# Kernel optimization log

Measured on AMD Instinct MI355X. Metric: run time of the kernel, lower is better.

Reference implementation:

```python
import jax, jax.numpy as jnp
import numpy as np

B, H, W = 64, 512, 512          # batch, image height/width
BH, BW = 8, 8                   # block_size
K = 256                         # n_blocks (codebook size)
L = BH * BW                     # block_len = 64
HT, WT = H // BH, W // BW       # tiles per axis
T = HT * WT                     # tiles_per_img = 4096
BETA = 35.0


def _unfold(img):
    # img: (B, 1, H, W) -> patches (B, T, L), matching torch.nn.Unfold
    # with kernel=stride=(BH,BW): tiles row-major, patch flattened (kh, kw).
    x = img.reshape(B, 1, HT, BH, WT, BW)
    x = x.transpose(0, 2, 4, 1, 3, 5)          # (B, HT, WT, 1, BH, BW)
    return x.reshape(B, T, L)


def _fold(patches):
    # patches: (B, T, L) -> img (B, 1, H, W); exact inverse of _unfold
    # (non-overlapping, so Fold is pure reassembly, no accumulation).
    x = patches.reshape(B, HT, WT, 1, BH, BW)
    x = x.transpose(0, 3, 1, 4, 2, 5)          # (B, 1, HT, BH, WT, BW)
    return x.reshape(B, 1, H, W)


def setup_inputs() -> dict:
    key = jax.random.key(0)
    k1, k2 = jax.random.split(key)
    target_img = jax.random.uniform(k1, (B, 1, H, W), dtype=jnp.float32)
    # Learned codebook parameter (Haar-ish init in the original; values
    # don't change the math being tested).
    blocks = jax.random.uniform(k2, (K, BH, BW), dtype=jnp.float32)
    return {"target_img": target_img, "blocks": blocks}


def reference(target_img, blocks):
    patches = _unfold(target_img).reshape(B * T, L)   # (N, L), N = B*T
    codes = blocks.reshape(K, L)                      # (K, L)

    # Squared distances ||a - b||^2 via the expanded form to avoid
    # materializing the (N, K, L) difference tensor.
    a2 = jnp.sum(patches * patches, axis=-1, keepdims=True)   # (N, 1)
    b2 = jnp.sum(codes * codes, axis=-1)                      # (K,)
    ab = patches @ codes.T                                    # (N, K)
    sqerr = a2 - 2.0 * ab + b2                                # (N, K)

    block_weights = jax.nn.softmax(-BETA * sqerr, axis=-1)    # (N, K)
    uf_reconstructed = block_weights @ codes                  # (N, L)

    reconstructed = _fold(uf_reconstructed.reshape(B, T, L))  # (B,1,H,W)
    choice_penalty = jnp.mean(
        jnp.minimum(block_weights, 1.0 - block_weights)) * K
    return reconstructed, choice_penalty
```

## Files before the change

kernel.cpp:

```cpp
#include <hip/hip_runtime.h>


typedef short short8 __attribute__((ext_vector_type(8)));
typedef float floatx4 __attribute__((ext_vector_type(4)));

namespace {
constexpr float BETA_C = 35.0f;
constexpr float TAU    = 1e-6f;
constexpr float INV_N  = 1.0f / 262144.0f;
constexpr size_t IMG_ELEMS = (size_t)64 * 512 * 512;
constexpr int WR = 0;
constexpr int WS = 4352;
constexpr int NWORDS = 4416;
}

__device__ __forceinline__ unsigned short f2bf(float x) {
  unsigned u = __float_as_uint(x);
  return (unsigned short)((u + 0x7FFFu + ((u >> 16) & 1u)) >> 16);
}
__device__ __forceinline__ float bf2f(unsigned short h) {
  return __uint_as_float((unsigned)h << 16);
}
__device__ __forceinline__ unsigned pack2(unsigned short lo, unsigned short hi) {
  return (unsigned)lo | ((unsigned)hi << 16);
}
__device__ __forceinline__ void cvt8t(float4 a, float4 b, short8& h, short8& l) {
  float f[8] = {a.x, a.y, a.z, a.w, b.x, b.y, b.z, b.w};
#pragma unroll
  for (int i = 0; i < 8; ++i) {
    unsigned short hh = f2bf(f[i]);
    h[i] = (short)hh;
    float lf = f[i] - bf2f(hh);
    l[i] = (short)(__float_as_uint(lf) >> 16);
  }
}
__device__ __forceinline__ int swz(int j) {
  return (j & ~7) | ((j ^ (j >> 3)) & 7);
}

__global__ void pack_codes(const float* __restrict__ blk,
                           unsigned* __restrict__ wsBh,
                           unsigned* __restrict__ wsBl,
                           float* __restrict__ wsB2) {
  const int c = threadIdx.x;
  const float* src = blk + c * 64;
  float b2 = 0.f;
#pragma unroll
  for (int g = 0; g < 8; ++g) {
#pragma unroll
    for (int t = 0; t < 4; ++t) {
      float v0 = src[g * 8 + 2 * t], v1 = src[g * 8 + 2 * t + 1];
      b2 += v0 * v0 + v1 * v1;
      unsigned short h0 = f2bf(v0), h1 = f2bf(v1);
      unsigned short l0 = f2bf(v0 - bf2f(h0)), l1 = f2bf(v1 - bf2f(h1));
      wsBh[(c * 8 + g) * 4 + t] = pack2(h0, h1);
      wsBl[(c * 8 + g) * 4 + t] = pack2(l0, l1);
    }
  }
  wsB2[c] = b2;
}

__global__ __launch_bounds__(256, 5) void recon_kernel(
    const float* __restrict__ img, const float* __restrict__ blk,
    const unsigned* __restrict__ wsBh, const unsigned* __restrict__ wsBl,
    const float* __restrict__ wsB2, float* __restrict__ out,
    float* __restrict__ penAcc) {
  __shared__ unsigned sMem[NWORDS];
  float* sMemF = reinterpret_cast<float*>(sMem);
  uint4* sMem4 = reinterpret_cast<uint4*>(sMem);

  const int tid = threadIdx.x;
  const int lane = tid & 63;
  const int wave = tid >> 6;
  const int b = blockIdx.x >> 6;
  const int ht = blockIdx.x & 63;
  const int c15 = lane & 15;
  const int q = lane >> 4;

  const float* imgBase = img + (size_t)b * (512 * 512) + (size_t)(ht * 8) * 512;
  const float* aptr = imgBase + q * 512 + (wave * 16 + c15) * 8;
  float4 v00 = *reinterpret_cast<const float4*>(aptr);
  float4 v01 = *reinterpret_cast<const float4*>(aptr + 4);
  float4 v10 = *reinterpret_cast<const float4*>(aptr + 2048);
  float4 v11 = *reinterpret_cast<const float4*>(aptr + 2048 + 4);

  uint4 tH[4], tL[4];
  {
    const uint4* src = reinterpret_cast<const uint4*>(wsBh);
#pragma unroll
    for (int i = 0; i < 4; ++i) tH[i] = src[swz(i * 256 + tid)];
  }

  short8 ah[2], al[2];
  cvt8t(v00, v01, ah[0], al[0]);
  cvt8t(v10, v11, ah[1], al[1]);

  const int kx = c15 & 7;
  const unsigned* pb0 = &sMem[(8 * c15 + (q ^ kx)) * 4];
  const unsigned* pb1 = &sMem[(8 * c15 + ((q ^ 4) ^ kx)) * 4];

  float m[4], sm[4];
  float rr[16] = {0.f, 0.f, 0.f, 0.f, 0.f, 0.f, 0.f, 0.f,
                  0.f, 0.f, 0.f, 0.f, 0.f, 0.f, 0.f, 0.f};

#pragma unroll
  for (int h = 0; h < 2; ++h) {
    if (h == 1) __syncthreads();
#pragma unroll
    for (int i = 0; i < 4; ++i) sMem4[i * 256 + tid] = tH[i];
    __syncthreads();
    {
      const uint4* src = reinterpret_cast<const uint4*>(wsBl) + h * 1024;
#pragma unroll
      for (int i = 0; i < 4; ++i) tL[i] = src[swz(i * 256 + tid)];
    }
    floatx4 acc[8];
#pragma unroll
    for (int n = 0; n < 8; ++n) acc[n] = (floatx4){0.f, 0.f, 0.f, 0.f};
#pragma unroll
    for (int n = 0; n < 8; ++n) {
      short8 b0 = *reinterpret_cast<const short8*>(pb0 + 512 * n);
      short8 b1 = *reinterpret_cast<const short8*>(pb1 + 512 * n);
      acc[n] = __builtin_amdgcn_mfma_f32_16x16x32_bf16(ah[0], b0, acc[n], 0, 0, 0);
      acc[n] = __builtin_amdgcn_mfma_f32_16x16x32_bf16(al[0], b0, acc[n], 0, 0, 0);
      acc[n] = __builtin_amdgcn_mfma_f32_16x16x32_bf16(ah[1], b1, acc[n], 0, 0, 0);
      acc[n] = __builtin_amdgcn_mfma_f32_16x16x32_bf16(al[1], b1, acc[n], 0, 0, 0);
    }
    __syncthreads();
#pragma unroll
    for (int i = 0; i < 4; ++i) sMem4[i * 256 + tid] = tL[i];
    __syncthreads();
    if (h == 0) {
      const uint4* src = reinterpret_cast<const uint4*>(wsBh) + 1024;
#pragma unroll
      for (int i = 0; i < 4; ++i) tH[i] = src[swz(i * 256 + tid)];
    }
#pragma unroll
    for (int n = 0; n < 8; ++n) {
      short8 b0 = *reinterpret_cast<const short8*>(pb0 + 512 * n);
      short8 b1 = *reinterpret_cast<const short8*>(pb1 + 512 * n);
      acc[n] = __builtin_amdgcn_mfma_f32_16x16x32_bf16(ah[0], b0, acc[n], 0, 0, 0);
      acc[n] = __builtin_amdgcn_mfma_f32_16x16x32_bf16(ah[1], b1, acc[n], 0, 0, 0);
    }

#pragma unroll
    for (int n = 0; n < 8; ++n) {
      float b2v = wsB2[128 * h + 16 * n + c15];
#pragma unroll
      for (int r = 0; r < 4; ++r)
        acc[n][r] = fmaf(2.0f * BETA_C, acc[n][r], -BETA_C * b2v);
    }
    float M[4];
#pragma unroll
    for (int r = 0; r < 4; ++r) {
      float mm = acc[0][r];
#pragma unroll
      for (int n = 1; n < 8; ++n) mm = fmaxf(mm, acc[n][r]);
#pragma unroll
      for (int off = 1; off <= 8; off <<= 1) mm = fmaxf(mm, __shfl_xor(mm, off, 64));
      M[r] = mm;
    }
    if (h == 0) {
#pragma unroll
      for (int r = 0; r < 4; ++r) { m[r] = M[r]; sm[r] = 0.f; }
    } else {
      float scl[4];
#pragma unroll
      for (int r = 0; r < 4; ++r) {
        float mn = fmaxf(m[r], M[r]);
        scl[r] = __expf(m[r] - mn);
        m[r] = mn;
        sm[r] *= scl[r];
      }
#pragma unroll
      for (int qq = 0; qq < 4; ++qq)
#pragma unroll
        for (int r = 0; r < 4; ++r) {
          float sq = __shfl(scl[r], qq * 16 + c15, 64);
          rr[4 * qq + r] *= sq;
        }
    }
#pragma unroll
    for (int n = 0; n < 8; ++n)
#pragma unroll
      for (int r = 0; r < 4; ++r) {
        float e = __expf(acc[n][r] - m[r]);
        acc[n][r] = e;
        sm[r] += e;
      }
#pragma unroll
    for (int n = 0; n < 8; ++n) {
      float em = fmaxf(fmaxf(acc[n][0], acc[n][1]), fmaxf(acc[n][2], acc[n][3]));
      unsigned long long msk = __ballot(em > TAU);
      while (msk) {
        int L = __builtin_ctzll(msk);
        msk &= msk - 1;
        float w0 = __uint_as_float(__builtin_amdgcn_readlane(__float_as_uint(acc[n][0]), L));
        float w1 = __uint_as_float(__builtin_amdgcn_readlane(__float_as_uint(acc[n][1]), L));
        float w2 = __uint_as_float(__builtin_amdgcn_readlane(__float_as_uint(acc[n][2]), L));
        float w3 = __uint_as_float(__builtin_amdgcn_readlane(__float_as_uint(acc[n][3]), L));
        float bv = blk[(size_t)(128 * h + 16 * n + (L & 15)) * 64 + lane];
        switch (L >> 4) {
          case 0: rr[0] += w0 * bv;  rr[1] += w1 * bv;  rr[2] += w2 * bv;  rr[3] += w3 * bv;  break;
          case 1: rr[4] += w0 * bv;  rr[5] += w1 * bv;  rr[6] += w2 * bv;  rr[7] += w3 * bv;  break;
          case 2: rr[8] += w0 * bv;  rr[9] += w1 * bv;  rr[10] += w2 * bv; rr[11] += w3 * bv; break;
          default: rr[12] += w0 * bv; rr[13] += w1 * bv; rr[14] += w2 * bv; rr[15] += w3 * bv; break;
        }
      }
    }
  }

  float invS[4];
#pragma unroll
  for (int r = 0; r < 4; ++r) {
#pragma unroll
    for (int off = 1; off <= 8; off <<= 1) sm[r] += __shfl_xor(sm[r], off, 64);
    invS[r] = 1.0f / sm[r];
  }
  float pen = 0.f;
  if (c15 == 0) {
#pragma unroll
    for (int r = 0; r < 4; ++r) {
      pen += (invS[r] > 0.5f) ? (2.0f - 2.0f * invS[r]) : 1.0f;
      sMemF[WS + wave * 16 + 4 * q + r] = invS[r];
    }
  }
  pen += __shfl_xor(pen, 16, 64);
  pen += __shfl_xor(pen, 32, 64);
  if (lane == 0) atomicAdd(penAcc, pen * INV_N);

  __syncthreads();

#pragma unroll
  for (int pl = 0; pl < 16; ++pl)
    sMemF[WR + (wave * 16 + pl) * 68 + lane] = rr[pl];
  float* outBase = out + (size_t)b * (512 * 512) + (size_t)(ht * 8) * 512 +
                   wave * 128;
#pragma unroll
  for (int i = 0; i < 4; ++i) {
    int f = i * 64 + lane;
    int row = f >> 5;
    int cc = f & 31;
    int wtl = cc >> 1, hw = cc & 1;
    float4 v = *reinterpret_cast<const float4*>(
        &sMemF[WR + (wave * 16 + wtl) * 68 + row * 8 + hw * 4]);
    float is = sMemF[WS + wave * 16 + wtl];
    v.x *= is; v.y *= is; v.z *= is; v.w *= is;
    *reinterpret_cast<float4*>(outBase + row * 512 + cc * 4) = v;
  }
}

extern "C" void kernel_launch(void* const* d_in, const int* in_sizes, int n_in,
                              void* d_out, int out_size, void* d_ws, size_t ws_size,
                              hipStream_t stream) {
  const float* img = (const float*)d_in[0];
  const float* blk = (const float*)d_in[1];
  float* out = (float*)d_out;
  float* penSlot = out + IMG_ELEMS;

  unsigned* wsBh = (unsigned*)d_ws;
  unsigned* wsBl = wsBh + 8192;
  float* wsB2 = (float*)(wsBl + 8192);

  pack_codes<<<dim3(1), dim3(256), 0, stream>>>(blk, wsBh, wsBl, wsB2);
  hipMemsetAsync(penSlot, 0, sizeof(float), stream);
  recon_kernel<<<dim3(4096), dim3(256), 0, stream>>>(img, blk, wsBh, wsBl,
                                                     wsB2, out, penSlot);
}
```

Before: 382.3 us.

## Stream codebook hi/lo halves directly into LDS with async global_load_lds

After: 347.2 us. 9.2% less time.

```diff
diff --git a/kernel.cpp b/kernel.cpp
--- a/kernel.cpp
+++ b/kernel.cpp
@@ -9,9 +9,11 @@
 constexpr float TAU    = 1e-6f;
 constexpr float INV_N  = 1.0f / 262144.0f;
 constexpr size_t IMG_ELEMS = (size_t)64 * 512 * 512;
-constexpr int WR = 0;
-constexpr int WS = 4352;
-constexpr int NWORDS = 4416;
+constexpr int WB0 = 0;
+constexpr int WB1 = 4096;
+constexpr int WR  = 0;
+constexpr int WS  = 4352;
+constexpr int NWORDS = 8192;
 }
 
 __device__ __forceinline__ unsigned short f2bf(float x) {
@@ -34,8 +36,10 @@
     l[i] = (short)(__float_as_uint(lf) >> 16);
   }
 }
-__device__ __forceinline__ int swz(int j) {
-  return (j & ~7) | ((j ^ (j >> 3)) & 7);
+__device__ __forceinline__ void cp16(const uint4* g, unsigned* l) {
+  __builtin_amdgcn_global_load_lds(
+      (const __attribute__((address_space(1))) void*)g,
+      (__attribute__((address_space(3))) void*)l, 16, 0, 0);
 }
 
 __global__ void pack_codes(const float* __restrict__ blk,
@@ -47,17 +51,18 @@
   float b2 = 0.f;
 #pragma unroll
   for (int g = 0; g < 8; ++g) {
+    int slot = c * 8 + (g ^ (c & 7));
 #pragma unroll
     for (int t = 0; t < 4; ++t) {
       float v0 = src[g * 8 + 2 * t], v1 = src[g * 8 + 2 * t + 1];
       b2 += v0 * v0 + v1 * v1;
       unsigned short h0 = f2bf(v0), h1 = f2bf(v1);
       unsigned short l0 = f2bf(v0 - bf2f(h0)), l1 = f2bf(v1 - bf2f(h1));
-      wsBh[(c * 8 + g) * 4 + t] = pack2(h0, h1);
-      wsBl[(c * 8 + g) * 4 + t] = pack2(l0, l1);
-    }
-  }
-  wsB2[c] = b2;
+      wsBh[slot * 4 + t] = pack2(h0, h1);
+      wsBl[slot * 4 + t] = pack2(l0, l1);
+    }
+  }
+  wsB2[c] = -BETA_C * b2;
 }
 
 __global__ __launch_bounds__(256, 5) void recon_kernel(
@@ -67,7 +72,6 @@
     float* __restrict__ penAcc) {
   __shared__ unsigned sMem[NWORDS];
   float* sMemF = reinterpret_cast<float*>(sMem);
-  uint4* sMem4 = reinterpret_cast<uint4*>(sMem);
 
   const int tid = threadIdx.x;
   const int lane = tid & 63;
@@ -84,17 +88,21 @@
   float4 v10 = *reinterpret_cast<const float4*>(aptr + 2048);
   float4 v11 = *reinterpret_cast<const float4*>(aptr + 2048 + 4);
 
-  uint4 tH[4], tL[4];
-  {
-    const uint4* src = reinterpret_cast<const uint4*>(wsBh);
-#pragma unroll
-    for (int i = 0; i < 4; ++i) tH[i] = src[swz(i * 256 + tid)];
+  const uint4* srcH = reinterpret_cast<const uint4*>(wsBh);
+  const uint4* srcL = reinterpret_cast<const uint4*>(wsBl);
+#pragma unroll
+  for (int i = 0; i < 4; ++i) {
+    cp16(srcH + i * 256 + tid, &sMem[WB0 + (i * 4 + wave) * 256]);
+    cp16(srcL + i * 256 + tid, &sMem[WB1 + (i * 4 + wave) * 256]);
   }
 
   short8 ah[2], al[2];
   cvt8t(v00, v01, ah[0], al[0]);
   cvt8t(v10, v11, ah[1], al[1]);
 
+  asm volatile("s_waitcnt vmcnt(0)" ::: "memory");
+  __syncthreads();
+
   const int kx = c15 & 7;
   const unsigned* pb0 = &sMem[(8 * c15 + (q ^ kx)) * 4];
   const unsigned* pb1 = &sMem[(8 * c15 + ((q ^ 4) ^ kx)) * 4];
@@ -105,50 +113,37 @@
 
 #pragma unroll
   for (int h = 0; h < 2; ++h) {
-    if (h == 1) __syncthreads();
-#pragma unroll
-    for (int i = 0; i < 4; ++i) sMem4[i * 256 + tid] = tH[i];
-    __syncthreads();
-    {
-      const uint4* src = reinterpret_cast<const uint4*>(wsBl) + h * 1024;
-#pragma unroll
-      for (int i = 0; i < 4; ++i) tL[i] = src[swz(i * 256 + tid)];
-    }
     floatx4 acc[8];
 #pragma unroll
     for (int n = 0; n < 8; ++n) acc[n] = (floatx4){0.f, 0.f, 0.f, 0.f};
 #pragma unroll
     for (int n = 0; n < 8; ++n) {
-      short8 b0 = *reinterpret_cast<const short8*>(pb0 + 512 * n);
-      short8 b1 = *reinterpret_cast<const short8*>(pb1 + 512 * n);
-      acc[n] = __builtin_amdgcn_mfma_f32_16x16x32_bf16(ah[0], b0, acc[n], 0, 0, 0);
-      acc[n] = __builtin_amdgcn_mfma_f32_16x16x32_bf16(al[0], b0, acc[n], 0, 0, 0);
-      acc[n] = __builtin_amdgcn_mfma_f32_16x16x32_bf16(ah[1], b1, acc[n], 0, 0, 0);
-      acc[n] = __builtin_amdgcn_mfma_f32_16x16x32_bf16(al[1], b1, acc[n], 0, 0, 0);
-    }
-    __syncthreads();
-#pragma unroll
-    for (int i = 0; i < 4; ++i) sMem4[i * 256 + tid] = tL[i];
-    __syncthreads();
+      short8 b0h = *reinterpret_cast<const short8*>(pb0 + 512 * n);
+      short8 b1h = *reinterpret_cast<const short8*>(pb1 + 512 * n);
+      short8 b0l = *reinterpret_cast<const short8*>(pb0 + WB1 + 512 * n);
+      short8 b1l = *reinterpret_cast<const short8*>(pb1 + WB1 + 512 * n);
+      acc[n] = __builtin_amdgcn_mfma_f32_16x16x32_bf16(ah[0], b0h, acc[n], 0, 0, 0);
+      acc[n] = __builtin_amdgcn_mfma_f32_16x16x32_bf16(al[0], b0h, acc[n], 0, 0, 0);
+      acc[n] = __builtin_amdgcn_mfma_f32_16x16x32_bf16(ah[1], b1h, acc[n], 0, 0, 0);
+      acc[n] = __builtin_amdgcn_mfma_f32_16x16x32_bf16(al[1], b1h, acc[n], 0, 0, 0);
+      acc[n] = __builtin_amdgcn_mfma_f32_16x16x32_bf16(ah[0], b0l, acc[n], 0, 0, 0);
+      acc[n] = __builtin_amdgcn_mfma_f32_16x16x32_bf16(ah[1], b1l, acc[n], 0, 0, 0);
+    }
     if (h == 0) {
-      const uint4* src = reinterpret_cast<const uint4*>(wsBh) + 1024;
-#pragma unroll
-      for (int i = 0; i < 4; ++i) tH[i] = src[swz(i * 256 + tid)];
-    }
+      __syncthreads();
+#pragma unroll
+      for (int i = 0; i < 4; ++i) {
+        cp16(srcH + 1024 + i * 256 + tid, &sMem[WB0 + (i * 4 + wave) * 256]);
+        cp16(srcL + 1024 + i * 256 + tid, &sMem[WB1 + (i * 4 + wave) * 256]);
+      }
+    }
+
 #pragma unroll
     for (int n = 0; n < 8; ++n) {
-      short8 b0 = *reinterpret_cast<const short8*>(pb0 + 512 * n);
-      short8 b1 = *reinterpret_cast<const short8*>(pb1 + 512 * n);
-      acc[n] = __builtin_amdgcn_mfma_f32_16x16x32_bf16(ah[0], b0, acc[n], 0, 0, 0);
-      acc[n] = __builtin_amdgcn_mfma_f32_16x16x32_bf16(ah[1], b1, acc[n], 0, 0, 0);
-    }
-
-#pragma unroll
-    for (int n = 0; n < 8; ++n) {
-      float b2v = wsB2[128 * h + 16 * n + c15];
+      float b2s = wsB2[128 * h + 16 * n + c15];
 #pragma unroll
       for (int r = 0; r < 4; ++r)
-        acc[n][r] = fmaf(2.0f * BETA_C, acc[n][r], -BETA_C * b2v);
+        acc[n][r] = fmaf(2.0f * BETA_C, acc[n][r], b2s);
     }
     float M[4];
 #pragma unroll
@@ -208,6 +203,10 @@
         }
       }
     }
+    if (h == 0) {
+      asm volatile("s_waitcnt vmcnt(0)" ::: "memory");
+      __syncthreads();
+    }
   }
 
   float invS[4];
@@ -220,10 +219,8 @@
   float pen = 0.f;
   if (c15 == 0) {
 #pragma unroll
-    for (int r = 0; r < 4; ++r) {
+    for (int r = 0; r < 4; ++r)
       pen += (invS[r] > 0.5f) ? (2.0f - 2.0f * invS[r]) : 1.0f;
-      sMemF[WS + wave * 16 + 4 * q + r] = invS[r];
-    }
   }
   pen += __shfl_xor(pen, 16, 64);
   pen += __shfl_xor(pen, 32, 64);
@@ -231,6 +228,11 @@
 
   __syncthreads();
 
+  if (c15 == 0) {
+#pragma unroll
+    for (int r = 0; r < 4; ++r)
+      sMemF[WS + wave * 16 + 4 * q + r] = invS[r];
+  }
 #pragma unroll
   for (int pl = 0; pl < 16; ++pl)
     sMemF[WR + (wave * 16 + pl) * 68 + lane] = rr[pl];
```
